# Optimization experiments

Measured on AMD Instinct MI355X. Metric: run time of the kernel, lower is better.

## Reference

```python
import jax, jax.numpy as jnp
import numpy as np

B, S, D, E, F = 2, 1024, 1024, 14, 2048

def setup_inputs() -> dict:
    key = jax.random.key(0)
    k0, k1, k2, k3 = jax.random.split(key, 4)
    h = jax.random.normal(k0, (B, S, D), jnp.float32)
    gate_w = jax.random.normal(k1, (E, D), jnp.float32) * 0.02
    # kaiming-uniform-ish scale for expert weights
    w1 = jax.random.normal(k2, (E, D, F), jnp.float32) * (1.0 / np.sqrt(D).astype(np.float32))
    b1 = jnp.zeros((E, F), jnp.float32)
    w2 = jax.random.normal(k3, (E, F, D), jnp.float32) * (1.0 / np.sqrt(F).astype(np.float32))
    b2 = jnp.zeros((E, D), jnp.float32)
    return {"h": h, "gate_w": gate_w, "w1": w1, "b1": b1, "w2": w2, "b2": b2}

def reference(h, gate_w, w1, b1, w2, b2):
    # Eval-mode forward (no expert dropout, router_step=None, return_aux=False path)
    Bb, Ss, Dd = h.shape
    x = h.reshape(Bb * Ss, Dd)                       # (N, D)
    logits = x @ gate_w.T                            # (N, E)
    probs = jax.nn.softmax(logits, axis=-1)
    top2_p, top2_i = jax.lax.top_k(probs, 2)         # (N, 2)
    w = top2_p / jnp.maximum(top2_p.sum(-1, keepdims=True), 1e-10)
    # dense all-experts FFN
    hh = jnp.einsum('nd,edf->nef', x, w1) + b1       # (N, E, F)
    hh = jax.nn.gelu(hh, approximate=False)          # torch F.gelu default = exact erf
    all_out = jnp.einsum('nef,efd->ned', hh, w2) + b2  # (N, E, D)
    n = jnp.arange(x.shape[0])
    out0 = all_out[n, top2_i[:, 0]]                  # (N, D)
    out1 = all_out[n, top2_i[:, 1]]
    moe_out = w[:, 0:1] * out0 + w[:, 1:2] * out1
    result = jnp.clip(x + moe_out, -100.0, 100.0).reshape(Bb, Ss, Dd)
    return result
```

## Files before the change

kernel.cpp:

```cpp
#include <hip/hip_runtime.h>
#include <cstdint>
#include <cstddef>

#define NTOK 2048
#define DDIM 1024
#define FDIM 2048
#define NEXP 14
#define MAXT 2048

typedef __attribute__((ext_vector_type(8))) short short8;
typedef __attribute__((ext_vector_type(4))) float floatx4;

__device__ __forceinline__ unsigned pack2bf(float lo, float hi) {
    unsigned a = __float_as_uint(lo), b = __float_as_uint(hi);
    return ((a + 0x8000u) >> 16) | ((b + 0x8000u) & 0xffff0000u);
}
__device__ __forceinline__ unsigned short f2bf1(float f) {
    return (unsigned short)((__float_as_uint(f) + 0x8000u) >> 16);
}

__device__ __forceinline__ void glds16(const void* g, void* lds) {
    __builtin_amdgcn_global_load_lds((const __attribute__((address_space(1))) unsigned*)g,
                                     (__attribute__((address_space(3))) unsigned*)lds, 16, 0, 0);
}

__global__ __launch_bounds__(256) void cvtx_kernel(const float* __restrict__ x,
                                                   unsigned short* __restrict__ xb,
                                                   int* __restrict__ cnt) {
    if (blockIdx.x == 0 && threadIdx.x < NEXP) cnt[threadIdx.x] = 0;
    const size_t i = ((size_t)blockIdx.x * 256 + threadIdx.x) * 8;
    float4 a = *(const float4*)(x + i);
    float4 b = *(const float4*)(x + i + 4);
    uint4 u;
    u.x = pack2bf(a.x, a.y); u.y = pack2bf(a.z, a.w);
    u.z = pack2bf(b.x, b.y); u.w = pack2bf(b.z, b.w);
    *(uint4*)(xb + i) = u;
}

__global__ __launch_bounds__(256) void gate_kernel(
    const float* __restrict__ x, const float* __restrict__ gw,
    int* __restrict__ cnt, int* __restrict__ lists, float* __restrict__ wt)
{
    const int wave = threadIdx.x >> 6, lane = threadIdx.x & 63;
    const int n = blockIdx.x * 4 + wave;
    float part[NEXP];
#pragma unroll
    for (int e = 0; e < NEXP; ++e) part[e] = 0.f;
    const float4* xr = (const float4*)(x + (size_t)n * DDIM);
#pragma unroll
    for (int kk = 0; kk < 4; ++kk) {
        const float4 xv = xr[kk * 64 + lane];
#pragma unroll
        for (int e = 0; e < NEXP; ++e) {
            const float4 g = ((const float4*)(gw + e * DDIM))[kk * 64 + lane];
            part[e] = fmaf(xv.x, g.x, fmaf(xv.y, g.y, fmaf(xv.z, g.z, fmaf(xv.w, g.w, part[e]))));
        }
    }
#pragma unroll
    for (int e = 0; e < NEXP; ++e) {
        float v = part[e];
        for (int off = 32; off; off >>= 1) v += __shfl_xor(v, off);
        part[e] = v;
    }
    int i0 = 0; float l0 = part[0];
#pragma unroll
    for (int e = 1; e < NEXP; ++e) if (part[e] > l0) { l0 = part[e]; i0 = e; }
    int i1 = -1; float l1 = -3.0e38f;
#pragma unroll
    for (int e = 0; e < NEXP; ++e) if (e != i0 && part[e] > l1) { l1 = part[e]; i1 = e; }
    if (lane == 0) {
        const float r  = __expf(l1 - l0);
        wt[2 * n]     = 1.f / (1.f + r);
        wt[2 * n + 1] = r / (1.f + r);
        int p0 = atomicAdd(&cnt[i0], 1); lists[i0 * MAXT + p0] = 2 * n;
        int p1 = atomicAdd(&cnt[i1], 1); lists[i1 * MAXT + p1] = 2 * n + 1;
    }
}

#define MAXJOBS 78
__global__ void jobs_kernel(const int* __restrict__ cnt, int* __restrict__ job_e,
                            int* __restrict__ job_mt, int* __restrict__ njobs) {
    if (threadIdx.x == 0) {
        int J = 0;
        for (int e = 0; e < NEXP; ++e) {
            const int m = (cnt[e] + 63) >> 6;
            for (int i = 0; i < m; ++i) { job_e[J] = e; job_mt[J] = i; ++J; }
        }
        njobs[0] = J;
    }
}

__global__ __launch_bounds__(256) void gemm1_kernel(
    const unsigned short* __restrict__ xb, const float* __restrict__ w1,
    const float* __restrict__ b1, const int* __restrict__ cnt,
    const int* __restrict__ lists, const int* __restrict__ job_e,
    const int* __restrict__ job_mt, const int* __restrict__ njobs,
    unsigned short* __restrict__ hh)
{
    const int j = blockIdx.y;
    if (j >= njobs[0]) return;
    const int e = job_e[j], mt = job_mt[j], nt = blockIdx.x;
    const int count = cnt[e];
    const int* list = lists + e * MAXT + mt * 64;
    const int mloc = min(64, count - mt * 64);

    __shared__ __align__(16) unsigned short As[2][64 * 32];
    __shared__ __align__(16) unsigned short Bs[2][128 * 32];

    const int t = threadIdx.x, lane = t & 63, wave = t >> 6;
    const int lrow = lane & 15, lq = lane >> 4;
    const int wn = wave * 32;

    const int arow = wave * 16 + (lane >> 2);
    const int atok = list[min(arow, mloc - 1)] >> 1;
    const unsigned short* aG = xb + (size_t)atok * DDIM + (lane & 3) * 8;
    const int bn = t & 127, bg = t >> 7;
    const float* bG = w1 + (size_t)e * DDIM * FDIM + nt * 128 + bn;

    floatx4 acc[4][2];
#pragma unroll
    for (int i = 0; i < 4; ++i)
#pragma unroll
        for (int jn = 0; jn < 2; ++jn) acc[i][jn] = (floatx4)0.f;

    float br[2][8];
    glds16(aG, &As[0][wave * 512]);
#pragma unroll
    for (int c = 0; c < 2; ++c) {
        const int kc = bg + 2 * c;
#pragma unroll
        for (int jj = 0; jj < 8; ++jj) br[c][jj] = bG[(size_t)(kc * 8 + jj) * FDIM];
    }
#pragma unroll
    for (int c = 0; c < 2; ++c) {
        const int kc = bg + 2 * c;
        uint4 u;
        u.x = pack2bf(br[c][0], br[c][1]); u.y = pack2bf(br[c][2], br[c][3]);
        u.z = pack2bf(br[c][4], br[c][5]); u.w = pack2bf(br[c][6], br[c][7]);
        *(uint4*)&Bs[0][bn * 32 + ((kc ^ (bn & 3)) * 8)] = u;
    }
#pragma unroll
    for (int c = 0; c < 2; ++c) {
        const int kc = bg + 2 * c;
#pragma unroll
        for (int jj = 0; jj < 8; ++jj) br[c][jj] = bG[(size_t)(32 + kc * 8 + jj) * FDIM];
    }

    int p = 0;
    for (int k0 = 0; k0 < DDIM; k0 += 32) {
        __syncthreads();
        if (k0 + 32 < DDIM) {
            glds16(aG + k0 + 32, &As[p ^ 1][wave * 512]);
#pragma unroll
            for (int c = 0; c < 2; ++c) {
                const int kc = bg + 2 * c;
                uint4 u;
                u.x = pack2bf(br[c][0], br[c][1]); u.y = pack2bf(br[c][2], br[c][3]);
                u.z = pack2bf(br[c][4], br[c][5]); u.w = pack2bf(br[c][6], br[c][7]);
                *(uint4*)&Bs[p ^ 1][bn * 32 + ((kc ^ (bn & 3)) * 8)] = u;
            }
        }
        if (k0 + 64 < DDIM) {
#pragma unroll
            for (int c = 0; c < 2; ++c) {
                const int kc = bg + 2 * c;
#pragma unroll
                for (int jj = 0; jj < 8; ++jj) br[c][jj] = bG[(size_t)(k0 + 64 + kc * 8 + jj) * FDIM];
            }
        }
        short8 af[4], bf[2];
#pragma unroll
        for (int i = 0; i < 4; ++i)
            af[i] = *(const short8*)&As[p][(i * 16 + lrow) * 32 + lq * 8];
#pragma unroll
        for (int jn = 0; jn < 2; ++jn) {
            const int n = wn + jn * 16 + lrow;
            bf[jn] = *(const short8*)&Bs[p][n * 32 + ((lq ^ (n & 3)) * 8)];
        }
#pragma unroll
        for (int i = 0; i < 4; ++i)
#pragma unroll
            for (int jn = 0; jn < 2; ++jn)
                acc[i][jn] = __builtin_amdgcn_mfma_f32_16x16x32_bf16(af[i], bf[jn], acc[i][jn], 0, 0, 0);
        p ^= 1;
    }
#pragma unroll
    for (int jn = 0; jn < 2; ++jn) {
        const int n = nt * 128 + wn + jn * 16 + lrow;
        const float bias = b1[e * FDIM + n];
#pragma unroll
        for (int i = 0; i < 4; ++i) {
#pragma unroll
            for (int r = 0; r < 4; ++r) {
                const int m = i * 16 + lq * 4 + r;
                if (m < mloc) {
                    const int pp = list[m];
                    float v = acc[i][jn][r] + bias;
                    v = 0.5f * v * (1.0f + erff(v * 0.70710678118654752f));
                    hh[(size_t)pp * FDIM + n] = f2bf1(v);
                }
            }
        }
    }
}

__global__ __launch_bounds__(256) void gemm2_kernel(
    const unsigned short* __restrict__ hh, const float* __restrict__ w2,
    const float* __restrict__ b2, const int* __restrict__ cnt,
    const int* __restrict__ lists, const int* __restrict__ job_e,
    const int* __restrict__ job_mt, const int* __restrict__ njobs,
    const float* __restrict__ wt, float* __restrict__ out0, float* __restrict__ out1)
{
    const int j = blockIdx.y;
    if (j >= njobs[0]) return;
    const int e = job_e[j], mt = job_mt[j], nt = blockIdx.x;
    const int count = cnt[e];
    const int* list = lists + e * MAXT + mt * 64;
    const int mloc = min(64, count - mt * 64);

    __shared__ __align__(16) unsigned short As[2][64 * 32];
    __shared__ __align__(16) unsigned short Bs[2][64 * 32];

    const int t = threadIdx.x, lane = t & 63, wave = t >> 6;
    const int lrow = lane & 15, lq = lane >> 4;
    const int wm = (wave & 1) * 32, wn = (wave >> 1) * 16;

    const int arow = wave * 16 + (lane >> 2);
    const int apair = list[min(arow, mloc - 1)];
    const unsigned short* aG = hh + (size_t)apair * FDIM + (lane & 3) * 8;
    const int bn = t & 63, bkc = t >> 6;
    const float* bG = w2 + (size_t)e * FDIM * DDIM + nt * 64 + bn;

    floatx4 acc[2][2];
#pragma unroll
    for (int i = 0; i < 2; ++i)
#pragma unroll
        for (int jn = 0; jn < 2; ++jn) acc[i][jn] = (floatx4)0.f;

    float br[8];
    glds16(aG, &As[0][wave * 512]);
#pragma unroll
    for (int jj = 0; jj < 8; ++jj) br[jj] = bG[(size_t)(bkc * 8 + jj) * DDIM];
    {
        uint4 u;
        u.x = pack2bf(br[0], br[1]); u.y = pack2bf(br[2], br[3]);
        u.z = pack2bf(br[4], br[5]); u.w = pack2bf(br[6], br[7]);
        *(uint4*)&Bs[0][bn * 32 + ((bkc ^ (bn & 3)) * 8)] = u;
    }
#pragma unroll
    for (int jj = 0; jj < 8; ++jj) br[jj] = bG[(size_t)(32 + bkc * 8 + jj) * DDIM];

    int p = 0;
    for (int k0 = 0; k0 < FDIM; k0 += 32) {
        __syncthreads();
        if (k0 + 32 < FDIM) {
            glds16(aG + k0 + 32, &As[p ^ 1][wave * 512]);
            uint4 u;
            u.x = pack2bf(br[0], br[1]); u.y = pack2bf(br[2], br[3]);
            u.z = pack2bf(br[4], br[5]); u.w = pack2bf(br[6], br[7]);
            *(uint4*)&Bs[p ^ 1][bn * 32 + ((bkc ^ (bn & 3)) * 8)] = u;
        }
        if (k0 + 64 < FDIM) {
#pragma unroll
            for (int jj = 0; jj < 8; ++jj) br[jj] = bG[(size_t)(k0 + 64 + bkc * 8 + jj) * DDIM];
        }
        short8 af[2], bf[2];
#pragma unroll
        for (int i = 0; i < 2; ++i)
            af[i] = *(const short8*)&As[p][(wm + i * 16 + lrow) * 32 + lq * 8];
#pragma unroll
        for (int jn = 0; jn < 2; ++jn) {
            const int n = wn + jn * 16 + lrow;
            bf[jn] = *(const short8*)&Bs[p][((wn * 2) + jn * 16 + lrow) * 32 + ((lq ^ (((wn * 2) + jn * 16 + lrow) & 3)) * 8)];
        }
#pragma unroll
        for (int i = 0; i < 2; ++i)
#pragma unroll
            for (int jn = 0; jn < 2; ++jn)
                acc[i][jn] = __builtin_amdgcn_mfma_f32_16x16x32_bf16(af[i], bf[jn], acc[i][jn], 0, 0, 0);
        p ^= 1;
    }
#pragma unroll
    for (int jn = 0; jn < 2; ++jn) {
        const int n = nt * 64 + (wn * 2) + jn * 16 + lrow;
        const float bias = b2[e * DDIM + n];
#pragma unroll
        for (int i = 0; i < 2; ++i) {
#pragma unroll
            for (int r = 0; r < 4; ++r) {
                const int m = wm + i * 16 + lq * 4 + r;
                if (m < mloc) {
                    const int pp = list[m];
                    const int tok = pp >> 1;
                    const float v = (acc[i][jn][r] + bias) * wt[pp];
                    float* dst = (pp & 1) ? out1 : out0;
                    dst[(size_t)tok * DDIM + n] = v;
                }
            }
        }
    }
}

__global__ __launch_bounds__(256) void finalize_kernel(
    const float* __restrict__ x, const float* __restrict__ o1,
    float* __restrict__ out)
{
    const size_t i = ((size_t)blockIdx.x * 256 + threadIdx.x) * 4;
    float4 xv = *(const float4*)(x + i);
    float4 a  = *(const float4*)(out + i);
    float4 b  = *(const float4*)(o1 + i);
    float4 r;
    r.x = fminf(fmaxf(xv.x + a.x + b.x, -100.f), 100.f);
    r.y = fminf(fmaxf(xv.y + a.y + b.y, -100.f), 100.f);
    r.z = fminf(fmaxf(xv.z + a.z + b.z, -100.f), 100.f);
    r.w = fminf(fmaxf(xv.w + a.w + b.w, -100.f), 100.f);
    *(float4*)(out + i) = r;
}

extern "C" void kernel_launch(void* const* d_in, const int* in_sizes, int n_in,
                              void* d_out, int out_size, void* d_ws, size_t ws_size,
                              hipStream_t stream) {
    const float* h  = (const float*)d_in[0];
    const float* gw = (const float*)d_in[1];
    const float* w1 = (const float*)d_in[2];
    const float* b1 = (const float*)d_in[3];
    const float* w2 = (const float*)d_in[4];
    const float* b2 = (const float*)d_in[5];
    float* out = (float*)d_out;

    char* ws = (char*)d_ws;
    int*   cnt    = (int*)ws;
    int*   lists  = (int*)(ws + 256);
    float* wt     = (float*)(ws + 114944);
    int*   job_e  = (int*)(ws + 131328);
    int*   job_mt = (int*)(ws + 131840);
    int*   njobs  = (int*)(ws + 132352);
    unsigned short* xb = (unsigned short*)(ws + 262144);
    float* o1     = (float*)(ws + 262144 + 4194304);
    unsigned short* hhb = (unsigned short*)(ws + 262144 + 4194304 + 8388608);

    cvtx_kernel<<<NTOK * DDIM / (256 * 8), 256, 0, stream>>>(h, xb, cnt);
    gate_kernel<<<NTOK / 4, 256, 0, stream>>>(h, gw, cnt, lists, wt);
    jobs_kernel<<<1, 64, 0, stream>>>(cnt, job_e, job_mt, njobs);
    gemm1_kernel<<<dim3(FDIM / 128, MAXJOBS), 256, 0, stream>>>(xb, w1, b1, cnt, lists, job_e, job_mt, njobs, hhb);
    gemm2_kernel<<<dim3(DDIM / 64, MAXJOBS), 256, 0, stream>>>(hhb, w2, b2, cnt, lists, job_e, job_mt, njobs, wt, out, o1);
    finalize_kernel<<<NTOK * DDIM / (256 * 4), 256, 0, stream>>>(h, o1, out);
}
```

Before: 431.9 us.

## Deepen K tile to 64, vectorize fp32 weight loads, widen gemm2 N tile

Both expert GEMMs now stage a 64-deep K slice per iteration instead of 32, halving barriers per K. The fp32 weight loads become float4 loads along N, with each thread packing four columns into bf16 and storing them through a new XOR swizzle. The warp layout changes to 2x2 with a 32x64 tile per wave. gemm2's N tile grows from 64 to 128, halving its grid and so re-reading each A row half as often. The larger LDS footprint (48KB) and more registers may lower occupancy.

```diff
diff --git a/kernel.cpp b/kernel.cpp
--- a/kernel.cpp
+++ b/kernel.cpp
@@ -23,6 +23,8 @@
     __builtin_amdgcn_global_load_lds((const __attribute__((address_space(1))) unsigned*)g,
                                      (__attribute__((address_space(3))) unsigned*)lds, 16, 0, 0);
 }
+
+__device__ __forceinline__ int bswz(int n) { return ((n >> 2) ^ n ^ (n >> 4)) & 7; }
 
 __global__ __launch_bounds__(256) void cvtx_kernel(const float* __restrict__ x,
                                                    unsigned short* __restrict__ xb,
@@ -104,95 +106,96 @@
     const int* list = lists + e * MAXT + mt * 64;
     const int mloc = min(64, count - mt * 64);
 
-    __shared__ __align__(16) unsigned short As[2][64 * 32];
-    __shared__ __align__(16) unsigned short Bs[2][128 * 32];
+    __shared__ __align__(16) unsigned short As[2][64 * 64];
+    __shared__ __align__(16) unsigned short Bs[2][128 * 64];
 
     const int t = threadIdx.x, lane = t & 63, wave = t >> 6;
     const int lrow = lane & 15, lq = lane >> 4;
-    const int wn = wave * 32;
-
-    const int arow = wave * 16 + (lane >> 2);
-    const int atok = list[min(arow, mloc - 1)] >> 1;
-    const unsigned short* aG = xb + (size_t)atok * DDIM + (lane & 3) * 8;
-    const int bn = t & 127, bg = t >> 7;
-    const float* bG = w1 + (size_t)e * DDIM * FDIM + nt * 128 + bn;
-
-    floatx4 acc[4][2];
-#pragma unroll
-    for (int i = 0; i < 4; ++i)
-#pragma unroll
-        for (int jn = 0; jn < 2; ++jn) acc[i][jn] = (floatx4)0.f;
-
-    float br[2][8];
-    glds16(aG, &As[0][wave * 512]);
-#pragma unroll
-    for (int c = 0; c < 2; ++c) {
-        const int kc = bg + 2 * c;
-#pragma unroll
-        for (int jj = 0; jj < 8; ++jj) br[c][jj] = bG[(size_t)(kc * 8 + jj) * FDIM];
-    }
-#pragma unroll
-    for (int c = 0; c < 2; ++c) {
-        const int kc = bg + 2 * c;
+    const int wm = (wave & 1) * 32, wn = (wave >> 1) * 64;
+
+    const int achk = (lane & 7) ^ (lane >> 3);
+    const int r0 = wave * 16 + (lane >> 3);
+    const unsigned short* aG0 = xb + (size_t)(list[min(r0, mloc - 1)] >> 1) * DDIM + achk * 8;
+    const unsigned short* aG1 = xb + (size_t)(list[min(r0 + 8, mloc - 1)] >> 1) * DDIM + achk * 8;
+
+    const int n4 = (t & 31) * 4, kg = t >> 5;
+    const float* bG = w1 + (size_t)e * DDIM * FDIM + nt * 128 + n4;
+
+    floatx4 acc[2][4];
+#pragma unroll
+    for (int i = 0; i < 2; ++i)
+#pragma unroll
+        for (int jn = 0; jn < 4; ++jn) acc[i][jn] = (floatx4)0.f;
+
+    floatx4 brv[8];
+    glds16(aG0, &As[0][(wave * 16) * 64]);
+    glds16(aG1, &As[0][(wave * 16 + 8) * 64]);
+#pragma unroll
+    for (int jj = 0; jj < 8; ++jj)
+        brv[jj] = *(const floatx4*)(bG + (size_t)(kg * 8 + jj) * FDIM);
+#pragma unroll
+    for (int nn = 0; nn < 4; ++nn) {
+        const int n = n4 + nn, slot = kg ^ bswz(n);
         uint4 u;
-        u.x = pack2bf(br[c][0], br[c][1]); u.y = pack2bf(br[c][2], br[c][3]);
-        u.z = pack2bf(br[c][4], br[c][5]); u.w = pack2bf(br[c][6], br[c][7]);
-        *(uint4*)&Bs[0][bn * 32 + ((kc ^ (bn & 3)) * 8)] = u;
-    }
-#pragma unroll
-    for (int c = 0; c < 2; ++c) {
-        const int kc = bg + 2 * c;
-#pragma unroll
-        for (int jj = 0; jj < 8; ++jj) br[c][jj] = bG[(size_t)(32 + kc * 8 + jj) * FDIM];
-    }
+        u.x = pack2bf(brv[0][nn], brv[1][nn]); u.y = pack2bf(brv[2][nn], brv[3][nn]);
+        u.z = pack2bf(brv[4][nn], brv[5][nn]); u.w = pack2bf(brv[6][nn], brv[7][nn]);
+        *(uint4*)&Bs[0][n * 64 + slot * 8] = u;
+    }
+#pragma unroll
+    for (int jj = 0; jj < 8; ++jj)
+        brv[jj] = *(const floatx4*)(bG + (size_t)(64 + kg * 8 + jj) * FDIM);
 
     int p = 0;
-    for (int k0 = 0; k0 < DDIM; k0 += 32) {
+    for (int k0 = 0; k0 < DDIM; k0 += 64) {
         __syncthreads();
-        if (k0 + 32 < DDIM) {
-            glds16(aG + k0 + 32, &As[p ^ 1][wave * 512]);
-#pragma unroll
-            for (int c = 0; c < 2; ++c) {
-                const int kc = bg + 2 * c;
+        if (k0 + 64 < DDIM) {
+            glds16(aG0 + k0 + 64, &As[p ^ 1][(wave * 16) * 64]);
+            glds16(aG1 + k0 + 64, &As[p ^ 1][(wave * 16 + 8) * 64]);
+#pragma unroll
+            for (int nn = 0; nn < 4; ++nn) {
+                const int n = n4 + nn, slot = kg ^ bswz(n);
                 uint4 u;
-                u.x = pack2bf(br[c][0], br[c][1]); u.y = pack2bf(br[c][2], br[c][3]);
-                u.z = pack2bf(br[c][4], br[c][5]); u.w = pack2bf(br[c][6], br[c][7]);
-                *(uint4*)&Bs[p ^ 1][bn * 32 + ((kc ^ (bn & 3)) * 8)] = u;
-            }
-        }
-        if (k0 + 64 < DDIM) {
-#pragma unroll
-            for (int c = 0; c < 2; ++c) {
-                const int kc = bg + 2 * c;
-#pragma unroll
-                for (int jj = 0; jj < 8; ++jj) br[c][jj] = bG[(size_t)(k0 + 64 + kc * 8 + jj) * FDIM];
-            }
-        }
-        short8 af[4], bf[2];
-#pragma unroll
-        for (int i = 0; i < 4; ++i)
-            af[i] = *(const short8*)&As[p][(i * 16 + lrow) * 32 + lq * 8];
-#pragma unroll
-        for (int jn = 0; jn < 2; ++jn) {
-            const int n = wn + jn * 16 + lrow;
-            bf[jn] = *(const short8*)&Bs[p][n * 32 + ((lq ^ (n & 3)) * 8)];
-        }
-#pragma unroll
-        for (int i = 0; i < 4; ++i)
-#pragma unroll
-            for (int jn = 0; jn < 2; ++jn)
-                acc[i][jn] = __builtin_amdgcn_mfma_f32_16x16x32_bf16(af[i], bf[jn], acc[i][jn], 0, 0, 0);
+                u.x = pack2bf(brv[0][nn], brv[1][nn]); u.y = pack2bf(brv[2][nn], brv[3][nn]);
+                u.z = pack2bf(brv[4][nn], brv[5][nn]); u.w = pack2bf(brv[6][nn], brv[7][nn]);
+                *(uint4*)&Bs[p ^ 1][n * 64 + slot * 8] = u;
+            }
+        }
+        if (k0 + 128 < DDIM) {
+#pragma unroll
+            for (int jj = 0; jj < 8; ++jj)
+                brv[jj] = *(const floatx4*)(bG + (size_t)(k0 + 128 + kg * 8 + jj) * FDIM);
+        }
+#pragma unroll
+        for (int ks = 0; ks < 2; ++ks) {
+            const int c = ks * 4 + lq;
+            short8 af[2], bf[4];
+#pragma unroll
+            for (int i = 0; i < 2; ++i) {
+                const int r = wm + i * 16 + lrow;
+                af[i] = *(const short8*)&As[p][r * 64 + ((c ^ (r & 7)) * 8)];
+            }
+#pragma unroll
+            for (int jn = 0; jn < 4; ++jn) {
+                const int n = wn + jn * 16 + lrow;
+                bf[jn] = *(const short8*)&Bs[p][n * 64 + ((c ^ bswz(n)) * 8)];
+            }
+#pragma unroll
+            for (int i = 0; i < 2; ++i)
+#pragma unroll
+                for (int jn = 0; jn < 4; ++jn)
+                    acc[i][jn] = __builtin_amdgcn_mfma_f32_16x16x32_bf16(af[i], bf[jn], acc[i][jn], 0, 0, 0);
+        }
         p ^= 1;
     }
 #pragma unroll
-    for (int jn = 0; jn < 2; ++jn) {
+    for (int jn = 0; jn < 4; ++jn) {
         const int n = nt * 128 + wn + jn * 16 + lrow;
         const float bias = b1[e * FDIM + n];
 #pragma unroll
-        for (int i = 0; i < 4; ++i) {
+        for (int i = 0; i < 2; ++i) {
 #pragma unroll
             for (int r = 0; r < 4; ++r) {
-                const int m = i * 16 + lq * 4 + r;
+                const int m = wm + i * 16 + lq * 4 + r;
                 if (m < mloc) {
                     const int pp = list[m];
                     float v = acc[i][jn][r] + bias;
@@ -218,71 +221,90 @@
     const int* list = lists + e * MAXT + mt * 64;
     const int mloc = min(64, count - mt * 64);
 
-    __shared__ __align__(16) unsigned short As[2][64 * 32];
-    __shared__ __align__(16) unsigned short Bs[2][64 * 32];
+    __shared__ __align__(16) unsigned short As[2][64 * 64];
+    __shared__ __align__(16) unsigned short Bs[2][128 * 64];
 
     const int t = threadIdx.x, lane = t & 63, wave = t >> 6;
     const int lrow = lane & 15, lq = lane >> 4;
-    const int wm = (wave & 1) * 32, wn = (wave >> 1) * 16;
-
-    const int arow = wave * 16 + (lane >> 2);
-    const int apair = list[min(arow, mloc - 1)];
-    const unsigned short* aG = hh + (size_t)apair * FDIM + (lane & 3) * 8;
-    const int bn = t & 63, bkc = t >> 6;
-    const float* bG = w2 + (size_t)e * FDIM * DDIM + nt * 64 + bn;
-
-    floatx4 acc[2][2];
+    const int wm = (wave & 1) * 32, wn = (wave >> 1) * 64;
+
+    const int achk = (lane & 7) ^ (lane >> 3);
+    const int r0 = wave * 16 + (lane >> 3);
+    const unsigned short* aG0 = hh + (size_t)list[min(r0, mloc - 1)] * FDIM + achk * 8;
+    const unsigned short* aG1 = hh + (size_t)list[min(r0 + 8, mloc - 1)] * FDIM + achk * 8;
+
+    const int n4 = (t & 31) * 4, kg = t >> 5;
+    const float* bG = w2 + (size_t)e * FDIM * DDIM + nt * 128 + n4;
+
+    floatx4 acc[2][4];
 #pragma unroll
     for (int i = 0; i < 2; ++i)
 #pragma unroll
-        for (int jn = 0; jn < 2; ++jn) acc[i][jn] = (floatx4)0.f;
-
-    float br[8];
-    glds16(aG, &As[0][wave * 512]);
-#pragma unroll
-    for (int jj = 0; jj < 8; ++jj) br[jj] = bG[(size_t)(bkc * 8 + jj) * DDIM];
-    {
+        for (int jn = 0; jn < 4; ++jn) acc[i][jn] = (floatx4)0.f;
+
+    floatx4 brv[8];
+    glds16(aG0, &As[0][(wave * 16) * 64]);
+    glds16(aG1, &As[0][(wave * 16 + 8) * 64]);
+#pragma unroll
+    for (int jj = 0; jj < 8; ++jj)
+        brv[jj] = *(const floatx4*)(bG + (size_t)(kg * 8 + jj) * DDIM);
+#pragma unroll
+    for (int nn = 0; nn < 4; ++nn) {
+        const int n = n4 + nn, slot = kg ^ bswz(n);
         uint4 u;
-        u.x = pack2bf(br[0], br[1]); u.y = pack2bf(br[2], br[3]);
-        u.z = pack2bf(br[4], br[5]); u.w = pack2bf(br[6], br[7]);
-        *(uint4*)&Bs[0][bn * 32 + ((bkc ^ (bn & 3)) * 8)] = u;
-    }
-#pragma unroll
-    for (int jj = 0; jj < 8; ++jj) br[jj] = bG[(size_t)(32 + bkc * 8 + jj) * DDIM];
+        u.x = pack2bf(brv[0][nn], brv[1][nn]); u.y = pack2bf(brv[2][nn], brv[3][nn]);
+        u.z = pack2bf(brv[4][nn], brv[5][nn]); u.w = pack2bf(brv[6][nn], brv[7][nn]);
+        *(uint4*)&Bs[0][n * 64 + slot * 8] = u;
+    }
+#pragma unroll
+    for (int jj = 0; jj < 8; ++jj)
+        brv[jj] = *(const floatx4*)(bG + (size_t)(64 + kg * 8 + jj) * DDIM);
 
     int p = 0;
-    for (int k0 = 0; k0 < FDIM; k0 += 32) {
+    for (int k0 = 0; k0 < FDIM; k0 += 64) {
         __syncthreads();
-        if (k0 + 32 < FDIM) {
-            glds16(aG + k0 + 32, &As[p ^ 1][wave * 512]);
-            uint4 u;
-            u.x = pack2bf(br[0], br[1]); u.y = pack2bf(br[2], br[3]);
-            u.z = pack2bf(br[4], br[5]); u.w = pack2bf(br[6], br[7]);
-            *(uint4*)&Bs[p ^ 1][bn * 32 + ((bkc ^ (bn & 3)) * 8)] = u;
-        }
         if (k0 + 64 < FDIM) {
-#pragma unroll
-            for (int jj = 0; jj < 8; ++jj) br[jj] = bG[(size_t)(k0 + 64 + bkc * 8 + jj) * DDIM];
-        }
-        short8 af[2], bf[2];
-#pragma unroll
-        for (int i = 0; i < 2; ++i)
-            af[i] = *(const short8*)&As[p][(wm + i * 16 + lrow) * 32 + lq * 8];
-#pragma unroll
-        for (int jn = 0; jn < 2; ++jn) {
-            const int n = wn + jn * 16 + lrow;
-            bf[jn] = *(const short8*)&Bs[p][((wn * 2) + jn * 16 + lrow) * 32 + ((lq ^ (((wn * 2) + jn * 16 + lrow) & 3)) * 8)];
-        }
-#pragma unroll
-        for (int i = 0; i < 2; ++i)
-#pragma unroll
-            for (int jn = 0; jn < 2; ++jn)
-                acc[i][jn] = __builtin_amdgcn_mfma_f32_16x16x32_bf16(af[i], bf[jn], acc[i][jn], 0, 0, 0);
+            glds16(aG0 + k0 + 64, &As[p ^ 1][(wave * 16) * 64]);
+            glds16(aG1 + k0 + 64, &As[p ^ 1][(wave * 16 + 8) * 64]);
+#pragma unroll
+            for (int nn = 0; nn < 4; ++nn) {
+                const int n = n4 + nn, slot = kg ^ bswz(n);
+                uint4 u;
+                u.x = pack2bf(brv[0][nn], brv[1][nn]); u.y = pack2bf(brv[2][nn], brv[3][nn]);
+                u.z = pack2bf(brv[4][nn], brv[5][nn]); u.w = pack2bf(brv[6][nn], brv[7][nn]);
+                *(uint4*)&Bs[p ^ 1][n * 64 + slot * 8] = u;
+            }
+        }
+        if (k0 + 128 < FDIM) {
+#pragma unroll
+            for (int jj = 0; jj < 8; ++jj)
+                brv[jj] = *(const floatx4*)(bG + (size_t)(k0 + 128 + kg * 8 + jj) * DDIM);
+        }
+#pragma unroll
+        for (int ks = 0; ks < 2; ++ks) {
+            const int c = ks * 4 + lq;
+            short8 af[2], bf[4];
+#pragma unroll
+            for (int i = 0; i < 2; ++i) {
+                const int r = wm + i * 16 + lrow;
+                af[i] = *(const short8*)&As[p][r * 64 + ((c ^ (r & 7)) * 8)];
+            }
+#pragma unroll
+            for (int jn = 0; jn < 4; ++jn) {
+                const int n = wn + jn * 16 + lrow;
+                bf[jn] = *(const short8*)&Bs[p][n * 64 + ((c ^ bswz(n)) * 8)];
+            }
+#pragma unroll
+            for (int i = 0; i < 2; ++i)
+#pragma unroll
+                for (int jn = 0; jn < 4; ++jn)
+                    acc[i][jn] = __builtin_amdgcn_mfma_f32_16x16x32_bf16(af[i], bf[jn], acc[i][jn], 0, 0, 0);
+        }
         p ^= 1;
     }
 #pragma unroll
-    for (int jn = 0; jn < 2; ++jn) {
-        const int n = nt * 64 + (wn * 2) + jn * 16 + lrow;
+    for (int jn = 0; jn < 4; ++jn) {
+        const int n = nt * 128 + wn + jn * 16 + lrow;
         const float bias = b2[e * DDIM + n];
 #pragma unroll
         for (int i = 0; i < 2; ++i) {
@@ -343,6 +365,6 @@
     gate_kernel<<<NTOK / 4, 256, 0, stream>>>(h, gw, cnt, lists, wt);
     jobs_kernel<<<1, 64, 0, stream>>>(cnt, job_e, job_mt, njobs);
     gemm1_kernel<<<dim3(FDIM / 128, MAXJOBS), 256, 0, stream>>>(xb, w1, b1, cnt, lists, job_e, job_mt, njobs, hhb);
-    gemm2_kernel<<<dim3(DDIM / 64, MAXJOBS), 256, 0, stream>>>(hhb, w2, b2, cnt, lists, job_e, job_mt, njobs, wt, out, o1);
+    gemm2_kernel<<<dim3(DDIM / 128, MAXJOBS), 256, 0, stream>>>(hhb, w2, b2, cnt, lists, job_e, job_mt, njobs, wt, out, o1);
     finalize_kernel<<<NTOK * DDIM / (256 * 4), 256, 0, stream>>>(h, o1, out);
 }
```

Measured after the change: 414.7 us. 1.04x faster.
